# Kernel optimization log

Measured on AMD Instinct MI355X. Metric: run time of the kernel, lower is better.

Reference implementation:

```python
import jax, jax.numpy as jnp
import numpy as np

B = 256        # graphs per batch
M = 512        # atoms per complex (uniform; batch = arange(N)//M)
K_NN = 33      # max_num_neighbors + 1 (loop=True includes self edge)
RADIUS = 5.0   # interaction_radius


def setup_inputs() -> dict:
    key = jax.random.key(0)
    # coords scaled so a 5 A radius keeps a realistic fraction of edges
    pos = jax.random.normal(key, (B * M, 3), dtype=jnp.float32) * 8.0
    batch = (jnp.arange(B * M, dtype=jnp.int32) // M).astype(jnp.int32)
    return {"pos": pos, "batch": batch}


def _safe_sqrt(x):
    # sqrt with well-defined value (and grad) at 0; forward-identical to sqrt
    pos_x = jnp.where(x > 0, x, 1.0)
    return jnp.where(x > 0, jnp.sqrt(pos_x), 0.0)


def reference(pos, batch):
    # batch is sorted with uniform graph size M, so grouping == reshape.
    p = pos.reshape(B, M, 3)
    sq = jnp.sum(p * p, axis=-1)                                  # [B, M]
    # squared pairwise distances per graph via ||x||^2+||y||^2-2xy
    d2 = sq[:, :, None] + sq[:, None, :] - 2.0 * jnp.einsum("bmd,bnd->bmn", p, p)
    d2 = jnp.maximum(d2, 0.0)                                     # [B, M, M]
    # k nearest (incl. self, d2=0) == knn_graph(pos, k, batch, loop=True)
    _, nbr = jax.lax.top_k(-d2, K_NN)                             # [B, M, K]
    base = (jnp.arange(B, dtype=jnp.int32) * M)[:, None, None]
    src = (nbr.astype(jnp.int32) + base).reshape(-1)              # neighbor (source) ids
    dst = jnp.repeat(jnp.arange(B * M, dtype=jnp.int32), K_NN)    # center (target) ids
    edge_index = jnp.stack([src, dst])                            # [2, B*M*K]
    # recompute distances on gathered endpoints, as the torch code does
    diff = pos[src] - pos[dst]                                    # [E, 3]
    dist = _safe_sqrt(jnp.sum(diff * diff, axis=-1))              # [E]
    mask = dist <= RADIUS                                         # radius filter (kept as mask: jit-static shapes)
    return edge_index, dist, mask
```

## Files before the change

kernel.cpp:

```cpp
#include <hip/hip_runtime.h>
#include <stdint.h>

#define BATCH    256
#define MPTS     512
#define KNN      33
#define RADIUS_F 5.0f
#define EDGES    (BATCH * MPTS * KNN)

#define BLOCKS_PER_GRAPH 8
#define ROWS_PER_BLOCK   64
#define THREADS          256
#define WAVES_PER_BLOCK  4
#define CAP              128
#define SLOT_STRIDE      (CAP + 2)

template <int J>
static __device__ __forceinline__ uint32_t shx32(uint32_t x) {
    if constexpr (J == 1)
        return (uint32_t)__builtin_amdgcn_update_dpp(0, (int)x, 0xB1, 0xF, 0xF, false);
    else if constexpr (J == 2)
        return (uint32_t)__builtin_amdgcn_update_dpp(0, (int)x, 0x4E, 0xF, 0xF, false);
    else if constexpr (J == 8)
        return (uint32_t)__builtin_amdgcn_update_dpp(0, (int)x, 0x128, 0xF, 0xF, false);
    else if constexpr (J == 4)
        return (uint32_t)__builtin_amdgcn_ds_swizzle((int)x, 0x101F);
    else if constexpr (J == 16)
        return (uint32_t)__builtin_amdgcn_ds_swizzle((int)x, 0x401F);
    else
        return (uint32_t)__shfl_xor((int)x, 32, 64);
}

template <int J>
static __device__ __forceinline__ uint64_t shx64(uint64_t v) {
    const uint32_t lo = shx32<J>((uint32_t)v);
    const uint32_t hi = shx32<J>((uint32_t)(v >> 32));
    return ((uint64_t)hi << 32) | (uint64_t)lo;
}

template <int J>
static __device__ __forceinline__ void ce_s(uint64_t& v, bool lowJ, bool up) {
    const uint64_t p = shx64<J>(v);
    const bool km = (lowJ == up);
    v = ((v < p) == km) ? v : p;
}

static __device__ __forceinline__ uint64_t bsort64(uint64_t v,
        bool b1, bool b2, bool b4, bool b8, bool b16, bool b32) {
    ce_s<1>(v, b1, b2);
    ce_s<2>(v, b2, b4);   ce_s<1>(v, b1, b4);
    ce_s<4>(v, b4, b8);   ce_s<2>(v, b2, b8);   ce_s<1>(v, b1, b8);
    ce_s<8>(v, b8, b16);  ce_s<4>(v, b4, b16);  ce_s<2>(v, b2, b16);  ce_s<1>(v, b1, b16);
    ce_s<16>(v, b16, b32); ce_s<8>(v, b8, b32); ce_s<4>(v, b4, b32);  ce_s<2>(v, b2, b32); ce_s<1>(v, b1, b32);
    ce_s<32>(v, b32, true); ce_s<16>(v, b16, true); ce_s<8>(v, b8, true);
    ce_s<4>(v, b4, true);   ce_s<2>(v, b2, true);   ce_s<1>(v, b1, true);
    return v;
}

static __device__ __forceinline__ void bsort128(uint64_t& v0, uint64_t& v1,
        bool b1, bool b2, bool b4, bool b8, bool b16, bool b32) {
    ce_s<1>(v0, b1, b2);   ce_s<1>(v1, b1, b2);
    ce_s<2>(v0, b2, b4);   ce_s<2>(v1, b2, b4);   ce_s<1>(v0, b1, b4);   ce_s<1>(v1, b1, b4);
    ce_s<4>(v0, b4, b8);   ce_s<4>(v1, b4, b8);   ce_s<2>(v0, b2, b8);   ce_s<2>(v1, b2, b8);
    ce_s<1>(v0, b1, b8);   ce_s<1>(v1, b1, b8);
    ce_s<8>(v0, b8, b16);  ce_s<8>(v1, b8, b16);  ce_s<4>(v0, b4, b16);  ce_s<4>(v1, b4, b16);
    ce_s<2>(v0, b2, b16);  ce_s<2>(v1, b2, b16);  ce_s<1>(v0, b1, b16);  ce_s<1>(v1, b1, b16);
    ce_s<16>(v0, b16, b32); ce_s<16>(v1, b16, b32); ce_s<8>(v0, b8, b32); ce_s<8>(v1, b8, b32);
    ce_s<4>(v0, b4, b32);   ce_s<4>(v1, b4, b32);   ce_s<2>(v0, b2, b32); ce_s<2>(v1, b2, b32);
    ce_s<1>(v0, b1, b32);   ce_s<1>(v1, b1, b32);
    ce_s<32>(v0, b32, true); ce_s<32>(v1, b32, false);
    ce_s<16>(v0, b16, true); ce_s<16>(v1, b16, false);
    ce_s<8>(v0, b8, true);   ce_s<8>(v1, b8, false);
    ce_s<4>(v0, b4, true);   ce_s<4>(v1, b4, false);
    ce_s<2>(v0, b2, true);   ce_s<2>(v1, b2, false);
    ce_s<1>(v0, b1, true);   ce_s<1>(v1, b1, false);
    {
        const bool sw = (v1 < v0);
        const uint64_t a = sw ? v1 : v0;
        const uint64_t b = sw ? v0 : v1;
        v0 = a; v1 = b;
    }
    ce_s<32>(v0, b32, true); ce_s<32>(v1, b32, true);
    ce_s<16>(v0, b16, true); ce_s<16>(v1, b16, true);
    ce_s<8>(v0, b8, true);   ce_s<8>(v1, b8, true);
    ce_s<4>(v0, b4, true);   ce_s<4>(v1, b4, true);
    ce_s<2>(v0, b2, true);   ce_s<2>(v1, b2, true);
    ce_s<1>(v0, b1, true);   ce_s<1>(v1, b1, true);
}

static __device__ __forceinline__ uint32_t wave_incl_scan(uint32_t x) {
    x += (uint32_t)__builtin_amdgcn_update_dpp(0, (int)x, 0x111, 0xF, 0xF, false);
    x += (uint32_t)__builtin_amdgcn_update_dpp(0, (int)x, 0x112, 0xF, 0xF, false);
    x += (uint32_t)__builtin_amdgcn_update_dpp(0, (int)x, 0x114, 0xF, 0xF, false);
    x += (uint32_t)__builtin_amdgcn_update_dpp(0, (int)x, 0x118, 0xF, 0xF, false);
    x += (uint32_t)__builtin_amdgcn_update_dpp(0, (int)x, 0x142, 0xA, 0xF, false);
    x += (uint32_t)__builtin_amdgcn_update_dpp(0, (int)x, 0x143, 0xC, 0xF, false);
    return x;
}

__global__ void __launch_bounds__(THREADS)
InteractionModule_50483045597845_kernel(const float* __restrict__ pos,
                                        float* __restrict__ out) {
    __shared__ float4 spt[MPTS];
    __shared__ uint64_t slots[WAVES_PER_BLOCK * 2][SLOT_STRIDE];

    const int graph = blockIdx.x / BLOCKS_PER_GRAPH;
    const int slice = blockIdx.x - graph * BLOCKS_PER_GRAPH;
    const int tid   = (int)threadIdx.x;

    for (int p = tid; p < MPTS; p += THREADS) {
        const float* pp = pos + (size_t)(graph * MPTS + p) * 3;
        const float x = pp[0], y = pp[1], z = pp[2];
        const float sq = __builtin_fmaf(x, x, __builtin_fmaf(y, y, __fmul_rn(z, z)));
        spt[p] = make_float4(x, y, z, sq);
    }
    __syncthreads();

    const int lane = tid & 63;
    const int wave = tid >> 6;

    const bool b1  = (lane & 1) == 0;
    const bool b2  = (lane & 2) == 0;
    const bool b4  = (lane & 4) == 0;
    const bool b8  = (lane & 8) == 0;
    const bool b16 = (lane & 16) == 0;
    const bool b32 = (lane & 32) == 0;

    auto doRow = [&](const uint32_t* sk, const float4 pc, int mRow, int region) {
        uint32_t h = sk[0];
        #pragma unroll
        for (int j = 1; j < 8; ++j) h = sk[j] < h ? sk[j] : h;

        uint32_t blo = 0u, bhi = 0x7FFFFFFFu;
        while (blo < bhi) {
            const uint32_t mid = (blo + bhi) >> 1;
            const int c = __popcll(__ballot(h <= mid));
            if (c < KNN) blo = mid + 1;
            else { bhi = mid; if (c <= KNN + 3) break; }
        }
        uint32_t P = bhi;

        uint32_t cnt = 0;
        #pragma unroll
        for (int j = 0; j < 8; ++j) cnt += (sk[j] <= P) ? 1u : 0u;
        uint32_t incl  = wave_incl_scan(cnt);
        uint32_t total = (uint32_t)__builtin_amdgcn_readlane((int)incl, 63);

        if (total > 64u) {
            while (blo < bhi) {
                const uint32_t mid = (blo + bhi) >> 1;
                const int c = __popcll(__ballot(h <= mid));
                if (c < KNN) blo = mid + 1; else bhi = mid;
            }
            P = bhi;
            cnt = 0;
            #pragma unroll
            for (int j = 0; j < 8; ++j) cnt += (sk[j] <= P) ? 1u : 0u;
            incl  = wave_incl_scan(cnt);
            total = (uint32_t)__builtin_amdgcn_readlane((int)incl, 63);
        }
        uint32_t dest = incl - cnt;

        slots[region][lane]      = ~0ull;
        slots[region][64 + lane] = ~0ull;

        #pragma unroll
        for (int j = 0; j < 8; ++j) {
            const bool     surv = (sk[j] <= P);
            const uint32_t d    = (surv && dest < (uint32_t)CAP) ? dest : (uint32_t)CAP;
            slots[region][d]    = ((uint64_t)sk[j] << 32) | (uint32_t)(lane | (j << 6));
            dest += surv ? 1u : 0u;
        }

        uint64_t v0 = slots[region][lane];
        if (total <= 64u) {
            v0 = bsort64(v0, b1, b2, b4, b8, b16, b32);
        } else {
            uint64_t v1 = slots[region][64 + lane];
            bsort128(v0, v1, b1, b2, b4, b8, b16, b32);
        }

        if (lane < KNN) {
            const int kept  = (int)((uint32_t)v0 & 0x1FFu);
            const float4 q  = spt[kept];
            const float dx  = __fsub_rn(q.x, pc.x);
            const float dy  = __fsub_rn(q.y, pc.y);
            const float dz  = __fsub_rn(q.z, pc.z);
            const float ss  = __fadd_rn(__fadd_rn(__fmul_rn(dx, dx),
                                                  __fmul_rn(dy, dy)),
                                        __fmul_rn(dz, dz));
            const float dist  = (ss > 0.0f) ? __fsqrt_rn(ss) : 0.0f;
            const float maskv = (dist <= RADIUS_F) ? 1.0f : 0.0f;
            const size_t e    = (size_t)mRow * KNN + (size_t)lane;
            out[e]                     = (float)(graph * MPTS + kept);
            out[(size_t)EDGES + e]     = (float)mRow;
            out[2 * (size_t)EDGES + e] = dist;
            out[3 * (size_t)EDGES + e] = maskv;
        }
    };

    #pragma unroll 1
    for (int it = 0; it < ROWS_PER_BLOCK / (WAVES_PER_BLOCK * 2); ++it) {
        const int mA = slice * ROWS_PER_BLOCK + it * (WAVES_PER_BLOCK * 2) + wave;
        const int mB = mA + WAVES_PER_BLOCK;

        const float4 pa = spt[mA];
        const float4 pb = spt[mB];

        uint32_t sA[8], sB[8];
        #pragma unroll
        for (int j = 0; j < 8; ++j) {
            const int n = lane + (j << 6);
            const float4 q = spt[n];
            const float dotA = __builtin_fmaf(pa.x, q.x,
                               __builtin_fmaf(pa.y, q.y, __fmul_rn(pa.z, q.z)));
            const float dotB = __builtin_fmaf(pb.x, q.x,
                               __builtin_fmaf(pb.y, q.y, __fmul_rn(pb.z, q.z)));
            float d2A = __builtin_fmaf(-2.0f, dotA, __fadd_rn(pa.w, q.w));
            float d2B = __builtin_fmaf(-2.0f, dotB, __fadd_rn(pb.w, q.w));
            d2A = fmaxf(d2A, 0.0f);
            d2B = fmaxf(d2B, 0.0f);
            sA[j] = (__float_as_uint(d2A) & 0xFFFFFFF8u) | (uint32_t)j;
            sB[j] = (__float_as_uint(d2B) & 0xFFFFFFF8u) | (uint32_t)j;
        }

        doRow(sA, pa, graph * MPTS + mA, wave);
        doRow(sB, pb, graph * MPTS + mB, wave + WAVES_PER_BLOCK);
    }
}

extern "C" void kernel_launch(void* const* d_in, const int* in_sizes, int n_in,
                              void* d_out, int out_size, void* d_ws, size_t ws_size,
                              hipStream_t stream) {
    (void)in_sizes; (void)n_in; (void)out_size; (void)d_ws; (void)ws_size;
    const float* pos = (const float*)d_in[0];
    float*       out = (float*)d_out;
    hipLaunchKernelGGL(InteractionModule_50483045597845_kernel,
                       dim3(BATCH * BLOCKS_PER_GRAPH), dim3(THREADS), 0, stream,
                       pos, out);
}
```

Before: 151.8 us.

## Interleave two rows' top-k selection and sort, use permlane swaps and packed FMA

Processes the two rows per wave jointly: their threshold binary searches run in one loop, and their candidate scatters and bitonic sorts are interleaved to expose instruction-level parallelism. In the common case where both rows keep at most 64 candidates, a fast path sorts both together. Rare overflow rows fall back to the old per-row tail. Lane exchanges at distances 16 and 32 switch to permlane swap builtins when the compiler provides them, and distance 4 switches to two DPP row shifts plus a select. The distance computation uses packed two-wide FMA. This adds register pressure and more complex control flow.

```diff
diff --git a/kernel.cpp b/kernel.cpp
--- a/kernel.cpp
+++ b/kernel.cpp
@@ -14,20 +14,47 @@
 #define CAP              128
 #define SLOT_STRIDE      (CAP + 2)
 
+typedef float f32x2 __attribute__((ext_vector_type(2)));
+
+#if defined(__has_builtin)
+#if __has_builtin(__builtin_amdgcn_permlane16_swap)
+#define HAVE_PL16 1
+#endif
+#if __has_builtin(__builtin_amdgcn_permlane32_swap)
+#define HAVE_PL32 1
+#endif
+#if __has_builtin(__builtin_elementwise_fma)
+#define HAVE_PKFMA 1
+#endif
+#endif
+
 template <int J>
 static __device__ __forceinline__ uint32_t shx32(uint32_t x) {
-    if constexpr (J == 1)
+    if constexpr (J == 1) {
         return (uint32_t)__builtin_amdgcn_update_dpp(0, (int)x, 0xB1, 0xF, 0xF, false);
-    else if constexpr (J == 2)
+    } else if constexpr (J == 2) {
         return (uint32_t)__builtin_amdgcn_update_dpp(0, (int)x, 0x4E, 0xF, 0xF, false);
-    else if constexpr (J == 8)
+    } else if constexpr (J == 4) {
+        const uint32_t a = (uint32_t)__builtin_amdgcn_update_dpp(0, (int)x, 0x104, 0xF, 0xF, false);
+        const uint32_t b = (uint32_t)__builtin_amdgcn_update_dpp(0, (int)x, 0x114, 0xF, 0xF, false);
+        return ((threadIdx.x & 4u) == 0u) ? a : b;
+    } else if constexpr (J == 8) {
         return (uint32_t)__builtin_amdgcn_update_dpp(0, (int)x, 0x128, 0xF, 0xF, false);
-    else if constexpr (J == 4)
-        return (uint32_t)__builtin_amdgcn_ds_swizzle((int)x, 0x101F);
-    else if constexpr (J == 16)
+    } else if constexpr (J == 16) {
+#ifdef HAVE_PL16
+        auto r = __builtin_amdgcn_permlane16_swap((int)x, (int)x, false, false);
+        return ((uint32_t)r[0] ^ (uint32_t)r[1]) ^ x;
+#else
         return (uint32_t)__builtin_amdgcn_ds_swizzle((int)x, 0x401F);
-    else
+#endif
+    } else {
+#ifdef HAVE_PL32
+        auto r = __builtin_amdgcn_permlane32_swap((int)x, (int)x, false, false);
+        return ((uint32_t)r[0] ^ (uint32_t)r[1]) ^ x;
+#else
         return (uint32_t)__shfl_xor((int)x, 32, 64);
+#endif
+    }
 }
 
 template <int J>
@@ -45,46 +72,59 @@
 }
 
 static __device__ __forceinline__ uint64_t bsort64(uint64_t v,
-        bool b1, bool b2, bool b4, bool b8, bool b16, bool b32) {
-    ce_s<1>(v, b1, b2);
-    ce_s<2>(v, b2, b4);   ce_s<1>(v, b1, b4);
-    ce_s<4>(v, b4, b8);   ce_s<2>(v, b2, b8);   ce_s<1>(v, b1, b8);
-    ce_s<8>(v, b8, b16);  ce_s<4>(v, b4, b16);  ce_s<2>(v, b2, b16);  ce_s<1>(v, b1, b16);
-    ce_s<16>(v, b16, b32); ce_s<8>(v, b8, b32); ce_s<4>(v, b4, b32);  ce_s<2>(v, b2, b32); ce_s<1>(v, b1, b32);
-    ce_s<32>(v, b32, true); ce_s<16>(v, b16, true); ce_s<8>(v, b8, true);
-    ce_s<4>(v, b4, true);   ce_s<2>(v, b2, true);   ce_s<1>(v, b1, true);
+        bool l1, bool l2, bool l4, bool l8, bool l16, bool l32) {
+    ce_s<1>(v, l1, l2);
+    ce_s<2>(v, l2, l4);   ce_s<1>(v, l1, l4);
+    ce_s<4>(v, l4, l8);   ce_s<2>(v, l2, l8);   ce_s<1>(v, l1, l8);
+    ce_s<8>(v, l8, l16);  ce_s<4>(v, l4, l16);  ce_s<2>(v, l2, l16);  ce_s<1>(v, l1, l16);
+    ce_s<16>(v, l16, l32); ce_s<8>(v, l8, l32); ce_s<4>(v, l4, l32);  ce_s<2>(v, l2, l32); ce_s<1>(v, l1, l32);
+    ce_s<32>(v, l32, true); ce_s<16>(v, l16, true); ce_s<8>(v, l8, true);
+    ce_s<4>(v, l4, true);   ce_s<2>(v, l2, true);   ce_s<1>(v, l1, true);
     return v;
 }
 
+static __device__ __forceinline__ void bsort64d(uint64_t& a, uint64_t& b,
+        bool l1, bool l2, bool l4, bool l8, bool l16, bool l32) {
+#define C2(J, L, U) do { ce_s<J>(a, L, U); ce_s<J>(b, L, U); } while (0)
+    C2(1, l1, l2);
+    C2(2, l2, l4);   C2(1, l1, l4);
+    C2(4, l4, l8);   C2(2, l2, l8);   C2(1, l1, l8);
+    C2(8, l8, l16);  C2(4, l4, l16);  C2(2, l2, l16);  C2(1, l1, l16);
+    C2(16, l16, l32); C2(8, l8, l32); C2(4, l4, l32);  C2(2, l2, l32); C2(1, l1, l32);
+    C2(32, l32, true); C2(16, l16, true); C2(8, l8, true);
+    C2(4, l4, true);   C2(2, l2, true);   C2(1, l1, true);
+#undef C2
+}
+
 static __device__ __forceinline__ void bsort128(uint64_t& v0, uint64_t& v1,
-        bool b1, bool b2, bool b4, bool b8, bool b16, bool b32) {
-    ce_s<1>(v0, b1, b2);   ce_s<1>(v1, b1, b2);
-    ce_s<2>(v0, b2, b4);   ce_s<2>(v1, b2, b4);   ce_s<1>(v0, b1, b4);   ce_s<1>(v1, b1, b4);
-    ce_s<4>(v0, b4, b8);   ce_s<4>(v1, b4, b8);   ce_s<2>(v0, b2, b8);   ce_s<2>(v1, b2, b8);
-    ce_s<1>(v0, b1, b8);   ce_s<1>(v1, b1, b8);
-    ce_s<8>(v0, b8, b16);  ce_s<8>(v1, b8, b16);  ce_s<4>(v0, b4, b16);  ce_s<4>(v1, b4, b16);
-    ce_s<2>(v0, b2, b16);  ce_s<2>(v1, b2, b16);  ce_s<1>(v0, b1, b16);  ce_s<1>(v1, b1, b16);
-    ce_s<16>(v0, b16, b32); ce_s<16>(v1, b16, b32); ce_s<8>(v0, b8, b32); ce_s<8>(v1, b8, b32);
-    ce_s<4>(v0, b4, b32);   ce_s<4>(v1, b4, b32);   ce_s<2>(v0, b2, b32); ce_s<2>(v1, b2, b32);
-    ce_s<1>(v0, b1, b32);   ce_s<1>(v1, b1, b32);
-    ce_s<32>(v0, b32, true); ce_s<32>(v1, b32, false);
-    ce_s<16>(v0, b16, true); ce_s<16>(v1, b16, false);
-    ce_s<8>(v0, b8, true);   ce_s<8>(v1, b8, false);
-    ce_s<4>(v0, b4, true);   ce_s<4>(v1, b4, false);
-    ce_s<2>(v0, b2, true);   ce_s<2>(v1, b2, false);
-    ce_s<1>(v0, b1, true);   ce_s<1>(v1, b1, false);
+        bool l1, bool l2, bool l4, bool l8, bool l16, bool l32) {
+    ce_s<1>(v0, l1, l2);   ce_s<1>(v1, l1, l2);
+    ce_s<2>(v0, l2, l4);   ce_s<2>(v1, l2, l4);   ce_s<1>(v0, l1, l4);   ce_s<1>(v1, l1, l4);
+    ce_s<4>(v0, l4, l8);   ce_s<4>(v1, l4, l8);   ce_s<2>(v0, l2, l8);   ce_s<2>(v1, l2, l8);
+    ce_s<1>(v0, l1, l8);   ce_s<1>(v1, l1, l8);
+    ce_s<8>(v0, l8, l16);  ce_s<8>(v1, l8, l16);  ce_s<4>(v0, l4, l16);  ce_s<4>(v1, l4, l16);
+    ce_s<2>(v0, l2, l16);  ce_s<2>(v1, l2, l16);  ce_s<1>(v0, l1, l16);  ce_s<1>(v1, l1, l16);
+    ce_s<16>(v0, l16, l32); ce_s<16>(v1, l16, l32); ce_s<8>(v0, l8, l32); ce_s<8>(v1, l8, l32);
+    ce_s<4>(v0, l4, l32);   ce_s<4>(v1, l4, l32);   ce_s<2>(v0, l2, l32); ce_s<2>(v1, l2, l32);
+    ce_s<1>(v0, l1, l32);   ce_s<1>(v1, l1, l32);
+    ce_s<32>(v0, l32, true); ce_s<32>(v1, l32, false);
+    ce_s<16>(v0, l16, true); ce_s<16>(v1, l16, false);
+    ce_s<8>(v0, l8, true);   ce_s<8>(v1, l8, false);
+    ce_s<4>(v0, l4, true);   ce_s<4>(v1, l4, false);
+    ce_s<2>(v0, l2, true);   ce_s<2>(v1, l2, false);
+    ce_s<1>(v0, l1, true);   ce_s<1>(v1, l1, false);
     {
         const bool sw = (v1 < v0);
         const uint64_t a = sw ? v1 : v0;
         const uint64_t b = sw ? v0 : v1;
         v0 = a; v1 = b;
     }
-    ce_s<32>(v0, b32, true); ce_s<32>(v1, b32, true);
-    ce_s<16>(v0, b16, true); ce_s<16>(v1, b16, true);
-    ce_s<8>(v0, b8, true);   ce_s<8>(v1, b8, true);
-    ce_s<4>(v0, b4, true);   ce_s<4>(v1, b4, true);
-    ce_s<2>(v0, b2, true);   ce_s<2>(v1, b2, true);
-    ce_s<1>(v0, b1, true);   ce_s<1>(v1, b1, true);
+    ce_s<32>(v0, l32, true); ce_s<32>(v1, l32, true);
+    ce_s<16>(v0, l16, true); ce_s<16>(v1, l16, true);
+    ce_s<8>(v0, l8, true);   ce_s<8>(v1, l8, true);
+    ce_s<4>(v0, l4, true);   ce_s<4>(v1, l4, true);
+    ce_s<2>(v0, l2, true);   ce_s<2>(v1, l2, true);
+    ce_s<1>(v0, l1, true);   ce_s<1>(v1, l1, true);
 }
 
 static __device__ __forceinline__ uint32_t wave_incl_scan(uint32_t x) {
@@ -118,67 +158,14 @@
     const int lane = tid & 63;
     const int wave = tid >> 6;
 
-    const bool b1  = (lane & 1) == 0;
-    const bool b2  = (lane & 2) == 0;
-    const bool b4  = (lane & 4) == 0;
-    const bool b8  = (lane & 8) == 0;
-    const bool b16 = (lane & 16) == 0;
-    const bool b32 = (lane & 32) == 0;
-
-    auto doRow = [&](const uint32_t* sk, const float4 pc, int mRow, int region) {
-        uint32_t h = sk[0];
-        #pragma unroll
-        for (int j = 1; j < 8; ++j) h = sk[j] < h ? sk[j] : h;
-
-        uint32_t blo = 0u, bhi = 0x7FFFFFFFu;
-        while (blo < bhi) {
-            const uint32_t mid = (blo + bhi) >> 1;
-            const int c = __popcll(__ballot(h <= mid));
-            if (c < KNN) blo = mid + 1;
-            else { bhi = mid; if (c <= KNN + 3) break; }
-        }
-        uint32_t P = bhi;
-
-        uint32_t cnt = 0;
-        #pragma unroll
-        for (int j = 0; j < 8; ++j) cnt += (sk[j] <= P) ? 1u : 0u;
-        uint32_t incl  = wave_incl_scan(cnt);
-        uint32_t total = (uint32_t)__builtin_amdgcn_readlane((int)incl, 63);
-
-        if (total > 64u) {
-            while (blo < bhi) {
-                const uint32_t mid = (blo + bhi) >> 1;
-                const int c = __popcll(__ballot(h <= mid));
-                if (c < KNN) blo = mid + 1; else bhi = mid;
-            }
-            P = bhi;
-            cnt = 0;
-            #pragma unroll
-            for (int j = 0; j < 8; ++j) cnt += (sk[j] <= P) ? 1u : 0u;
-            incl  = wave_incl_scan(cnt);
-            total = (uint32_t)__builtin_amdgcn_readlane((int)incl, 63);
-        }
-        uint32_t dest = incl - cnt;
-
-        slots[region][lane]      = ~0ull;
-        slots[region][64 + lane] = ~0ull;
-
-        #pragma unroll
-        for (int j = 0; j < 8; ++j) {
-            const bool     surv = (sk[j] <= P);
-            const uint32_t d    = (surv && dest < (uint32_t)CAP) ? dest : (uint32_t)CAP;
-            slots[region][d]    = ((uint64_t)sk[j] << 32) | (uint32_t)(lane | (j << 6));
-            dest += surv ? 1u : 0u;
-        }
-
-        uint64_t v0 = slots[region][lane];
-        if (total <= 64u) {
-            v0 = bsort64(v0, b1, b2, b4, b8, b16, b32);
-        } else {
-            uint64_t v1 = slots[region][64 + lane];
-            bsort128(v0, v1, b1, b2, b4, b8, b16, b32);
-        }
-
+    const bool l1  = (lane & 1) == 0;
+    const bool l2  = (lane & 2) == 0;
+    const bool l4  = (lane & 4) == 0;
+    const bool l8  = (lane & 8) == 0;
+    const bool l16 = (lane & 16) == 0;
+    const bool l32 = (lane & 32) == 0;
+
+    auto emitRow = [&](uint64_t v0, const float4 pc, int mRow) {
         if (lane < KNN) {
             const int kept  = (int)((uint32_t)v0 & 0x1FFu);
             const float4 q  = spt[kept];
@@ -198,6 +185,43 @@
         }
     };
 
+    auto doTail = [&](const uint32_t* sk, uint32_t h, uint32_t P,
+                      uint32_t incl, uint32_t cnt, uint32_t total,
+                      const float4 pc, int mRow, int region) {
+        if (total > 64u) {
+            uint32_t lo = 0u, hi = P;
+            while (lo < hi) {
+                const uint32_t mid = (lo + hi) >> 1;
+                const int c = __popcll(__ballot(h <= mid));
+                if (c < KNN) lo = mid + 1; else hi = mid;
+            }
+            P = hi;
+            cnt = 0;
+            #pragma unroll
+            for (int j = 0; j < 8; ++j) cnt += (sk[j] <= P) ? 1u : 0u;
+            incl  = wave_incl_scan(cnt);
+            total = (uint32_t)__builtin_amdgcn_readlane((int)incl, 63);
+        }
+        uint32_t dest = incl - cnt;
+        slots[region][lane]      = ~0ull;
+        slots[region][64 + lane] = ~0ull;
+        #pragma unroll
+        for (int j = 0; j < 8; ++j) {
+            const bool surv = (sk[j] <= P);
+            if (surv && dest < (uint32_t)CAP)
+                slots[region][dest] = ((uint64_t)sk[j] << 32) | (uint32_t)(lane | (j << 6));
+            dest += surv ? 1u : 0u;
+        }
+        uint64_t v0 = slots[region][lane];
+        if (total <= 64u) {
+            v0 = bsort64(v0, l1, l2, l4, l8, l16, l32);
+        } else {
+            uint64_t v1 = slots[region][64 + lane];
+            bsort128(v0, v1, l1, l2, l4, l8, l16, l32);
+        }
+        emitRow(v0, pc, mRow);
+    };
+
     #pragma unroll 1
     for (int it = 0; it < ROWS_PER_BLOCK / (WAVES_PER_BLOCK * 2); ++it) {
         const int mA = slice * ROWS_PER_BLOCK + it * (WAVES_PER_BLOCK * 2) + wave;
@@ -207,24 +231,104 @@
         const float4 pb = spt[mB];
 
         uint32_t sA[8], sB[8];
+        {
+#ifdef HAVE_PKFMA
+            const f32x2 px = {pa.x, pb.x}, py = {pa.y, pb.y};
+            const f32x2 pz = {pa.z, pb.z}, pw = {pa.w, pb.w};
+            const f32x2 m2 = {-2.0f, -2.0f};
+#endif
+            #pragma unroll
+            for (int j = 0; j < 8; ++j) {
+                const int n = lane + (j << 6);
+                const float4 q = spt[n];
+#ifdef HAVE_PKFMA
+                const f32x2 qx = {q.x, q.x}, qy = {q.y, q.y};
+                const f32x2 qz = {q.z, q.z}, qw = {q.w, q.w};
+                const f32x2 dot = __builtin_elementwise_fma(px, qx,
+                                  __builtin_elementwise_fma(py, qy, pz * qz));
+                const f32x2 d2  = __builtin_elementwise_fma(m2, dot, pw + qw);
+                const float d2A = fmaxf(d2[0], 0.0f);
+                const float d2B = fmaxf(d2[1], 0.0f);
+#else
+                const float dotA = __builtin_fmaf(pa.x, q.x,
+                                   __builtin_fmaf(pa.y, q.y, __fmul_rn(pa.z, q.z)));
+                const float dotB = __builtin_fmaf(pb.x, q.x,
+                                   __builtin_fmaf(pb.y, q.y, __fmul_rn(pb.z, q.z)));
+                const float d2A = fmaxf(__builtin_fmaf(-2.0f, dotA, __fadd_rn(pa.w, q.w)), 0.0f);
+                const float d2B = fmaxf(__builtin_fmaf(-2.0f, dotB, __fadd_rn(pb.w, q.w)), 0.0f);
+#endif
+                sA[j] = (__float_as_uint(d2A) & 0xFFFFFFF8u) | (uint32_t)j;
+                sB[j] = (__float_as_uint(d2B) & 0xFFFFFFF8u) | (uint32_t)j;
+            }
+        }
+
+        uint32_t hA = sA[0], hB = sB[0];
+        #pragma unroll
+        for (int j = 1; j < 8; ++j) {
+            hA = sA[j] < hA ? sA[j] : hA;
+            hB = sB[j] < hB ? sB[j] : hB;
+        }
+
+        uint32_t loA = 0u, hiA_ = 0x7FFFFFFFu;
+        uint32_t loB = 0u, hiB_ = 0x7FFFFFFFu;
+        while (loA < hiA_ || loB < hiB_) {
+            const uint32_t midA = (loA + hiA_) >> 1;
+            const uint32_t midB = (loB + hiB_) >> 1;
+            const int cA = __popcll(__ballot(hA <= midA));
+            const int cB = __popcll(__ballot(hB <= midB));
+            const bool openA = loA < hiA_, okA = cA >= KNN;
+            const bool openB = loB < hiB_, okB = cB >= KNN;
+            const uint32_t nloA = okA ? ((cA <= KNN + 3) ? midA : loA) : (midA + 1u);
+            const uint32_t nloB = okB ? ((cB <= KNN + 3) ? midB : loB) : (midB + 1u);
+            const uint32_t nhiA = okA ? midA : hiA_;
+            const uint32_t nhiB = okB ? midB : hiB_;
+            loA = openA ? nloA : loA;  hiA_ = openA ? nhiA : hiA_;
+            loB = openB ? nloB : loB;  hiB_ = openB ? nhiB : hiB_;
+        }
+        const uint32_t PA = hiA_;
+        const uint32_t PB = hiB_;
+
+        uint32_t cntA = 0, cntB = 0;
         #pragma unroll
         for (int j = 0; j < 8; ++j) {
-            const int n = lane + (j << 6);
-            const float4 q = spt[n];
-            const float dotA = __builtin_fmaf(pa.x, q.x,
-                               __builtin_fmaf(pa.y, q.y, __fmul_rn(pa.z, q.z)));
-            const float dotB = __builtin_fmaf(pb.x, q.x,
-                               __builtin_fmaf(pb.y, q.y, __fmul_rn(pb.z, q.z)));
-            float d2A = __builtin_fmaf(-2.0f, dotA, __fadd_rn(pa.w, q.w));
-            float d2B = __builtin_fmaf(-2.0f, dotB, __fadd_rn(pb.w, q.w));
-            d2A = fmaxf(d2A, 0.0f);
-            d2B = fmaxf(d2B, 0.0f);
-            sA[j] = (__float_as_uint(d2A) & 0xFFFFFFF8u) | (uint32_t)j;
-            sB[j] = (__float_as_uint(d2B) & 0xFFFFFFF8u) | (uint32_t)j;
-        }
-
-        doRow(sA, pa, graph * MPTS + mA, wave);
-        doRow(sB, pb, graph * MPTS + mB, wave + WAVES_PER_BLOCK);
+            cntA += (sA[j] <= PA) ? 1u : 0u;
+            cntB += (sB[j] <= PB) ? 1u : 0u;
+        }
+        const uint32_t inclA = wave_incl_scan(cntA);
+        const uint32_t inclB = wave_incl_scan(cntB);
+        const uint32_t totalA = (uint32_t)__builtin_amdgcn_readlane((int)inclA, 63);
+        const uint32_t totalB = (uint32_t)__builtin_amdgcn_readlane((int)inclB, 63);
+
+        const int rA = wave;
+        const int rB = wave + WAVES_PER_BLOCK;
+        const int mRowA = graph * MPTS + mA;
+        const int mRowB = graph * MPTS + mB;
+
+        if (__builtin_expect(totalA > 64u || totalB > 64u, 0)) {
+            doTail(sA, hA, PA, inclA, cntA, totalA, pa, mRowA, rA);
+            doTail(sB, hB, PB, inclB, cntB, totalB, pb, mRowB, rB);
+        } else {
+            slots[rA][lane] = ~0ull;
+            slots[rB][lane] = ~0ull;
+            uint32_t dA = inclA - cntA;
+            uint32_t dB = inclB - cntB;
+            #pragma unroll
+            for (int j = 0; j < 8; ++j) {
+                const bool svA = (sA[j] <= PA);
+                const bool svB = (sB[j] <= PB);
+                const uint32_t wA_ = svA ? dA : (64u + (uint32_t)lane);
+                const uint32_t wB_ = svB ? dB : (64u + (uint32_t)lane);
+                slots[rA][wA_] = ((uint64_t)sA[j] << 32) | (uint32_t)(lane | (j << 6));
+                slots[rB][wB_] = ((uint64_t)sB[j] << 32) | (uint32_t)(lane | (j << 6));
+                dA += svA ? 1u : 0u;
+                dB += svB ? 1u : 0u;
+            }
+            uint64_t vA = slots[rA][lane];
+            uint64_t vB = slots[rB][lane];
+            bsort64d(vA, vB, l1, l2, l4, l8, l16, l32);
+            emitRow(vA, pa, mRowA);
+            emitRow(vB, pb, mRowB);
+        }
     }
 }
 
```

Result: slower. 165.4 us (+9.0%).
